# Kernel tuning notes

Measured on AMD Instinct MI355X. Metric: run time of the kernel, lower is better.

The kernel has to match this reference:

```python
import jax, jax.numpy as jnp
import numpy as np

B, N, K, D = 16, 8192, 20, 64  # batch, points, neighbors, feature dim
LN_EPS = 1e-5


def setup_inputs() -> dict:
    key = jax.random.key(0)
    k1, k2, k3 = jax.random.split(key, 3)
    x = jax.random.normal(k1, (B, N, D), dtype=jnp.float32)
    neighbor_ind = jax.random.randint(k2, (B, N, K), 0, N)
    # torch Linear(2D -> D, bias=False): weight shape (out=D, in=2D), y = feat @ W.T
    W = jax.random.normal(k3, (D, 2 * D), dtype=jnp.float32) * (1.0 / np.sqrt(2 * D))
    gamma = jnp.ones((D,), jnp.float32)
    beta = jnp.zeros((D,), jnp.float32)
    return {"x": x, "neighbor_ind": neighbor_ind, "W": W, "gamma": gamma, "beta": beta}


def reference(x, neighbor_ind, W, gamma, beta):
    # route(): gather neighbor features and build [neighbor - center, center]
    neighbor_x = jax.vmap(lambda xb, ib: xb[ib])(x, neighbor_ind)        # (b, n, k, d)
    center = x[:, :, None, :]                                            # (b, n, 1, d)
    feat = jnp.concatenate(
        [neighbor_x - center, jnp.broadcast_to(center, neighbor_x.shape)], axis=-1
    )                                                                    # (b, n, k, 2d)
    # per-edge Linear (bias=False), then max over k neighbors
    h = jnp.einsum('bnke,oe->bnko', feat, W)                             # (b, n, k, d)
    h = h.max(axis=2)                                                    # (b, n, d)
    # LayerNorm over last dim, then exact GELU
    mu = h.mean(axis=-1, keepdims=True)
    var = jnp.mean((h - mu) ** 2, axis=-1, keepdims=True)
    hn = (h - mu) * jax.lax.rsqrt(var + LN_EPS) * gamma + beta
    return jax.nn.gelu(hn, approximate=False)
```

## Files before the change

### kernel.cpp

```cpp
#include <hip/hip_runtime.h>
#include <math.h>

#define B_ 16
#define N_ 8192
#define K_ 20
#define NPTS (B_ * N_)

typedef __attribute__((ext_vector_type(4))) float f4;
typedef __attribute__((ext_vector_type(8))) short s8;
typedef __attribute__((ext_vector_type(4))) unsigned int u4;
typedef __attribute__((ext_vector_type(4))) unsigned short us4;

__device__ __forceinline__ unsigned short f2bf(float f) {
    union { float f; unsigned u; } v; v.f = f;
    return (unsigned short)((v.u + 0x7FFFu + ((v.u >> 16) & 1u)) >> 16);
}
__device__ __forceinline__ float bfhi(unsigned w) { return __uint_as_float(w & 0xFFFF0000u); }
__device__ __forceinline__ float bflo(unsigned w) { return __uint_as_float(w << 16); }

__global__ __launch_bounds__(256) void prep_kernel(const float* __restrict__ W,
                                                   unsigned short* __restrict__ Wg) {
    const int i = blockIdx.x * 256 + threadIdx.x;
    const int j = i >> 6, d = i & 63;
    const float v = (j < 64) ? W[j * 128 + d]
                             : (W[(j - 64) * 128 + 64 + d] - W[(j - 64) * 128 + d]);
    Wg[i] = f2bf(v);
}

__global__ __launch_bounds__(256) void proj_kernel(const float* __restrict__ x,
                                                   const unsigned short* __restrict__ Wg,
                                                   unsigned short* __restrict__ Y1,
                                                   unsigned short* __restrict__ Bs) {
    __shared__ unsigned short Wl[128 * 72];
    const int t = threadIdx.x;

    for (int i = t; i < 1024; i += 256) {
        u4 v = ((const u4*)Wg)[i];
        *((u4*)((char*)Wl + (i >> 3) * 144 + (i & 7) * 16)) = v;
    }
    __syncthreads();

    const int lane = t & 63;
    const int wv = t >> 6;
    const int m = lane & 15;
    const int q = lane >> 4;
    const int pbase = blockIdx.x * 64 + wv * 16;

    const float* xr = x + (size_t)(pbase + m) * 64 + q * 8;
    f4 x0 = *(const f4*)(xr);
    f4 x1 = *(const f4*)(xr + 4);
    f4 x2 = *(const f4*)(xr + 32);
    f4 x3 = *(const f4*)(xr + 36);
    s8 X0, X1;
    X0[0]=(short)f2bf(x0.x); X0[1]=(short)f2bf(x0.y); X0[2]=(short)f2bf(x0.z); X0[3]=(short)f2bf(x0.w);
    X0[4]=(short)f2bf(x1.x); X0[5]=(short)f2bf(x1.y); X0[6]=(short)f2bf(x1.z); X0[7]=(short)f2bf(x1.w);
    X1[0]=(short)f2bf(x2.x); X1[1]=(short)f2bf(x2.y); X1[2]=(short)f2bf(x2.z); X1[3]=(short)f2bf(x2.w);
    X1[4]=(short)f2bf(x3.x); X1[5]=(short)f2bf(x3.y); X1[6]=(short)f2bf(x3.z); X1[7]=(short)f2bf(x3.w);

    f4 acc[8];
#pragma unroll
    for (int tt = 0; tt < 8; ++tt) acc[tt] = (f4)0.f;

#pragma unroll
    for (int s = 0; s < 2; ++s) {
        const s8 X = s ? X1 : X0;
#pragma unroll
        for (int tt = 0; tt < 8; ++tt) {
            s8 w = *(const s8*)((const char*)Wl + (16 * tt + m) * 144 + s * 64 + q * 16);
            acc[tt] = __builtin_amdgcn_mfma_f32_16x16x32_bf16(w, X, acc[tt], 0, 0, 0);
        }
    }

    const size_t prow = (size_t)(pbase + m) * 64;
#pragma unroll
    for (int tt = 0; tt < 4; ++tt) {
        us4 u;
        u.x = f2bf(acc[tt][0]); u.y = f2bf(acc[tt][1]);
        u.z = f2bf(acc[tt][2]); u.w = f2bf(acc[tt][3]);
        *(us4*)&Y1[prow + tt * 16 + q * 4] = u;
    }
#pragma unroll
    for (int tt = 4; tt < 8; ++tt) {
        us4 u;
        u.x = f2bf(acc[tt][0]); u.y = f2bf(acc[tt][1]);
        u.z = f2bf(acc[tt][2]); u.w = f2bf(acc[tt][3]);
        *(us4*)&Bs[prow + (tt - 4) * 16 + q * 4] = u;
    }
}

__global__ __launch_bounds__(256) void gather_kernel(const unsigned short* __restrict__ Y1,
                                                     const unsigned short* __restrict__ Bs,
                                                     const int* __restrict__ ind,
                                                     const float* __restrict__ gamma,
                                                     const float* __restrict__ beta,
                                                     float* __restrict__ out) {
    const int lane = threadIdx.x & 63;
    const int wave = threadIdx.x >> 6;
    const int sub = lane & 7;
    const int q = lane >> 3;
    const int bi = blockIdx.x;
    const int bt = bi & 15;
    const int jj = bi >> 4;
    const int p = bt * N_ + jj * 32 + wave * 8 + q;
    const int bbase = bt * N_ * 64;

    int idxs[K_];
    const int4* ip = (const int4*)&ind[p * K_];
#pragma unroll
    for (int v = 0; v < 5; ++v) {
        int4 iv = ip[v];
        idxs[4 * v + 0] = iv.x; idxs[4 * v + 1] = iv.y;
        idxs[4 * v + 2] = iv.z; idxs[4 * v + 3] = iv.w;
    }

    f4 ma = (f4)(-INFINITY), mb = (f4)(-INFINITY);
#pragma unroll
    for (int r = 0; r < 2; ++r) {
        u4 rv[10];
#pragma unroll
        for (int k = 0; k < 10; ++k)
            rv[k] = *(const u4*)(Y1 + bbase + idxs[r * 10 + k] * 64 + sub * 8);
#pragma unroll
        for (int k = 0; k < 10; ++k) {
            ma.x = fmaxf(ma.x, bflo(rv[k].x)); ma.y = fmaxf(ma.y, bfhi(rv[k].x));
            ma.z = fmaxf(ma.z, bflo(rv[k].y)); ma.w = fmaxf(ma.w, bfhi(rv[k].y));
            mb.x = fmaxf(mb.x, bflo(rv[k].z)); mb.y = fmaxf(mb.y, bfhi(rv[k].z));
            mb.z = fmaxf(mb.z, bflo(rv[k].w)); mb.w = fmaxf(mb.w, bfhi(rv[k].w));
        }
    }

    u4 bsv = __builtin_nontemporal_load((const u4*)(Bs + (size_t)p * 64 + sub * 8));
    f4 ha, hb;
    ha.x = ma.x + bflo(bsv.x); ha.y = ma.y + bfhi(bsv.x);
    ha.z = ma.z + bflo(bsv.y); ha.w = ma.w + bfhi(bsv.y);
    hb.x = mb.x + bflo(bsv.z); hb.y = mb.y + bfhi(bsv.z);
    hb.z = mb.z + bflo(bsv.w); hb.w = mb.w + bfhi(bsv.w);

    float s = ha.x + ha.y + ha.z + ha.w + hb.x + hb.y + hb.z + hb.w;
#pragma unroll
    for (int off = 4; off >= 1; off >>= 1) s += __shfl_xor(s, off, 64);
    const float mu = s * (1.0f / 64.0f);
    f4 da = ha - mu, db = hb - mu;
    float v2 = da.x * da.x + da.y * da.y + da.z * da.z + da.w * da.w
             + db.x * db.x + db.y * db.y + db.z * db.z + db.w * db.w;
#pragma unroll
    for (int off = 4; off >= 1; off >>= 1) v2 += __shfl_xor(v2, off, 64);
    const float rstd = rsqrtf(v2 * (1.0f / 64.0f) + 1e-5f);

    const f4 g0 = *(const f4*)&gamma[sub * 8];
    const f4 g1 = *(const f4*)&gamma[sub * 8 + 4];
    const f4 b0 = *(const f4*)&beta[sub * 8];
    const f4 b1 = *(const f4*)&beta[sub * 8 + 4];
    f4 na = da * rstd * g0 + b0;
    f4 nb = db * rstd * g1 + b1;

    f4 r0, r1;
    r0.x = 0.5f * na.x * (1.0f + erff(na.x * 0.70710678f));
    r0.y = 0.5f * na.y * (1.0f + erff(na.y * 0.70710678f));
    r0.z = 0.5f * na.z * (1.0f + erff(na.z * 0.70710678f));
    r0.w = 0.5f * na.w * (1.0f + erff(na.w * 0.70710678f));
    r1.x = 0.5f * nb.x * (1.0f + erff(nb.x * 0.70710678f));
    r1.y = 0.5f * nb.y * (1.0f + erff(nb.y * 0.70710678f));
    r1.z = 0.5f * nb.z * (1.0f + erff(nb.z * 0.70710678f));
    r1.w = 0.5f * nb.w * (1.0f + erff(nb.w * 0.70710678f));
    float* op = &out[(size_t)p * 64 + sub * 8];
    __builtin_nontemporal_store(r0, (f4*)op);
    __builtin_nontemporal_store(r1, (f4*)(op + 4));
}

extern "C" void kernel_launch(void* const* d_in, const int* in_sizes, int n_in,
                              void* d_out, int out_size, void* d_ws, size_t ws_size,
                              hipStream_t stream) {
    const float* x     = (const float*)d_in[0];
    const int*   ind   = (const int*)d_in[1];
    const float* W     = (const float*)d_in[2];
    const float* gamma = (const float*)d_in[3];
    const float* beta  = (const float*)d_in[4];
    float* out = (float*)d_out;

    unsigned short* Bs = (unsigned short*)d_ws;
    unsigned short* Y1 = Bs + (size_t)NPTS * 64;
    unsigned short* Wg = Y1 + (size_t)NPTS * 64;

    prep_kernel<<<32, 256, 0, stream>>>(W, Wg);
    proj_kernel<<<NPTS / 64, 256, 0, stream>>>(x, Wg, Y1, Bs);
    gather_kernel<<<NPTS / 32, 256, 0, stream>>>(Y1, Bs, ind, gamma, beta, out);
}
```

Before: 125.6 us.

## Fuse prep, projection and gather into one cooperative persistent kernel

Replaces the three launches with one cooperative kernel of 512 blocks. Each block builds the bf16 weight fragments in registers, projects 256 points, keeps the center term in shared memory, and writes only the neighbor table Y1 to global memory. A grid-wide sync then lets the same block gather, max-reduce (using v_max3), LayerNorm and apply GELU for its points. This removes two launch gaps and the global round trip of the center term, at the cost of a grid barrier and fewer resident blocks. The old three-kernel path is kept as a fallback if the cooperative launch fails.

New measurement: 216.3 us. 72.1% more time.

```diff
diff --git a/kernel.cpp b/kernel.cpp
--- a/kernel.cpp
+++ b/kernel.cpp
@@ -1,4 +1,5 @@
 #include <hip/hip_runtime.h>
+#include <hip/hip_cooperative_groups.h>
 #include <math.h>
 
 #define B_ 16
@@ -10,6 +11,7 @@
 typedef __attribute__((ext_vector_type(8))) short s8;
 typedef __attribute__((ext_vector_type(4))) unsigned int u4;
 typedef __attribute__((ext_vector_type(4))) unsigned short us4;
+typedef __attribute__((ext_vector_type(4))) int i4;
 
 __device__ __forceinline__ unsigned short f2bf(float f) {
     union { float f; unsigned u; } v; v.f = f;
@@ -17,6 +19,181 @@
 }
 __device__ __forceinline__ float bfhi(unsigned w) { return __uint_as_float(w & 0xFFFF0000u); }
 __device__ __forceinline__ float bflo(unsigned w) { return __uint_as_float(w << 16); }
+__device__ __forceinline__ float max3f(float a, float b, float c) {
+    float d;
+    asm("v_max3_f32 %0, %1, %2, %3" : "=v"(d) : "v"(a), "v"(b), "v"(c));
+    return d;
+}
+
+__global__ __launch_bounds__(256, 3) void fused_kernel(
+    const float* __restrict__ x, const int* __restrict__ ind,
+    const float* __restrict__ W, const float* __restrict__ gamma,
+    const float* __restrict__ beta, float* __restrict__ out,
+    unsigned short* __restrict__ Y1)
+{
+    __shared__ unsigned short BsL[256 * 72];
+
+    const int t = threadIdx.x;
+    const int lane = t & 63, wv = t >> 6;
+    const int g = blockIdx.x;
+    const int b = (g & 7) + 8 * ((g >> 3) & 1);
+    const int z = g >> 4;
+    const int p0 = b * N_ + z * 256;
+
+    const int mm = lane & 15, qq = lane >> 4;
+    s8 wf[16];
+#pragma unroll
+    for (int tt = 0; tt < 8; ++tt) {
+#pragma unroll
+        for (int s = 0; s < 2; ++s) {
+            const int k0 = s * 32 + qq * 8;
+            s8 w;
+            if (tt < 4) {
+                const int row = 16 * tt + mm;
+                f4 a0 = *(const f4*)&W[row * 128 + k0];
+                f4 a1 = *(const f4*)&W[row * 128 + k0 + 4];
+                w[0]=(short)f2bf(a0.x); w[1]=(short)f2bf(a0.y);
+                w[2]=(short)f2bf(a0.z); w[3]=(short)f2bf(a0.w);
+                w[4]=(short)f2bf(a1.x); w[5]=(short)f2bf(a1.y);
+                w[6]=(short)f2bf(a1.z); w[7]=(short)f2bf(a1.w);
+            } else {
+                const int row = 16 * (tt - 4) + mm;
+                f4 a0 = *(const f4*)&W[row * 128 + 64 + k0];
+                f4 a1 = *(const f4*)&W[row * 128 + 64 + k0 + 4];
+                f4 c0 = *(const f4*)&W[row * 128 + k0];
+                f4 c1 = *(const f4*)&W[row * 128 + k0 + 4];
+                w[0]=(short)f2bf(a0.x-c0.x); w[1]=(short)f2bf(a0.y-c0.y);
+                w[2]=(short)f2bf(a0.z-c0.z); w[3]=(short)f2bf(a0.w-c0.w);
+                w[4]=(short)f2bf(a1.x-c1.x); w[5]=(short)f2bf(a1.y-c1.y);
+                w[6]=(short)f2bf(a1.z-c1.z); w[7]=(short)f2bf(a1.w-c1.w);
+            }
+            wf[tt * 2 + s] = w;
+        }
+    }
+
+#pragma unroll 2
+    for (int tile = 0; tile < 4; ++tile) {
+        const int plocal = tile * 64 + wv * 16 + mm;
+        const int pg = p0 + plocal;
+        const float* xr = x + (size_t)pg * 64 + qq * 8;
+        f4 x0 = __builtin_nontemporal_load((const f4*)xr);
+        f4 x1 = __builtin_nontemporal_load((const f4*)(xr + 4));
+        f4 x2 = __builtin_nontemporal_load((const f4*)(xr + 32));
+        f4 x3 = __builtin_nontemporal_load((const f4*)(xr + 36));
+        s8 X0, X1;
+        X0[0]=(short)f2bf(x0.x); X0[1]=(short)f2bf(x0.y); X0[2]=(short)f2bf(x0.z); X0[3]=(short)f2bf(x0.w);
+        X0[4]=(short)f2bf(x1.x); X0[5]=(short)f2bf(x1.y); X0[6]=(short)f2bf(x1.z); X0[7]=(short)f2bf(x1.w);
+        X1[0]=(short)f2bf(x2.x); X1[1]=(short)f2bf(x2.y); X1[2]=(short)f2bf(x2.z); X1[3]=(short)f2bf(x2.w);
+        X1[4]=(short)f2bf(x3.x); X1[5]=(short)f2bf(x3.y); X1[6]=(short)f2bf(x3.z); X1[7]=(short)f2bf(x3.w);
+
+        f4 acc[8];
+#pragma unroll
+        for (int tt = 0; tt < 8; ++tt) acc[tt] = (f4)0.f;
+#pragma unroll
+        for (int s = 0; s < 2; ++s) {
+            const s8 X = s ? X1 : X0;
+#pragma unroll
+            for (int tt = 0; tt < 8; ++tt)
+                acc[tt] = __builtin_amdgcn_mfma_f32_16x16x32_bf16(wf[tt * 2 + s], X, acc[tt], 0, 0, 0);
+        }
+
+        const size_t prow = (size_t)pg * 64;
+#pragma unroll
+        for (int tt = 0; tt < 4; ++tt) {
+            us4 u;
+            u.x = f2bf(acc[tt][0]); u.y = f2bf(acc[tt][1]);
+            u.z = f2bf(acc[tt][2]); u.w = f2bf(acc[tt][3]);
+            __builtin_nontemporal_store(u, (us4*)&Y1[prow + tt * 16 + qq * 4]);
+        }
+#pragma unroll
+        for (int tt = 4; tt < 8; ++tt) {
+            us4 u;
+            u.x = f2bf(acc[tt][0]); u.y = f2bf(acc[tt][1]);
+            u.z = f2bf(acc[tt][2]); u.w = f2bf(acc[tt][3]);
+            *(us4*)((char*)BsL + plocal * 144 + (tt - 4) * 32 + qq * 8) = u;
+        }
+    }
+
+    cooperative_groups::this_grid().sync();
+
+    const int sub = lane & 7;
+    const int qp = lane >> 3;
+    const f4 g0 = *(const f4*)&gamma[sub * 8];
+    const f4 g1 = *(const f4*)&gamma[sub * 8 + 4];
+    const f4 be0 = *(const f4*)&beta[sub * 8];
+    const f4 be1 = *(const f4*)&beta[sub * 8 + 4];
+    const unsigned short* tbl = Y1 + (size_t)b * (N_ * 64) + sub * 8;
+
+#pragma unroll 1
+    for (int pass = 0; pass < 8; ++pass) {
+        const int pl = pass * 32 + wv * 8 + qp;
+        const int pg = p0 + pl;
+
+        int idxs[K_];
+        const i4* ip = (const i4*)&ind[pg * K_];
+#pragma unroll
+        for (int v = 0; v < 5; ++v) {
+            i4 iv = __builtin_nontemporal_load(ip + v);
+            idxs[4 * v + 0] = iv.x; idxs[4 * v + 1] = iv.y;
+            idxs[4 * v + 2] = iv.z; idxs[4 * v + 3] = iv.w;
+        }
+
+        f4 ma = (f4)(-INFINITY), mb = (f4)(-INFINITY);
+#pragma unroll
+        for (int r = 0; r < 2; ++r) {
+            u4 rv[10];
+#pragma unroll
+            for (int k = 0; k < 10; ++k)
+                rv[k] = *(const u4*)(tbl + idxs[r * 10 + k] * 64);
+#pragma unroll
+            for (int k = 0; k < 10; k += 2) {
+                u4 a = rv[k], c = rv[k + 1];
+                ma.x = max3f(ma.x, bflo(a.x), bflo(c.x));
+                ma.y = max3f(ma.y, bfhi(a.x), bfhi(c.x));
+                ma.z = max3f(ma.z, bflo(a.y), bflo(c.y));
+                ma.w = max3f(ma.w, bfhi(a.y), bfhi(c.y));
+                mb.x = max3f(mb.x, bflo(a.z), bflo(c.z));
+                mb.y = max3f(mb.y, bfhi(a.z), bfhi(c.z));
+                mb.z = max3f(mb.z, bflo(a.w), bflo(c.w));
+                mb.w = max3f(mb.w, bfhi(a.w), bfhi(c.w));
+            }
+        }
+
+        const u4 bsv = *(const u4*)((const char*)BsL + pl * 144 + sub * 16);
+        f4 ha, hb;
+        ha.x = ma.x + bflo(bsv.x); ha.y = ma.y + bfhi(bsv.x);
+        ha.z = ma.z + bflo(bsv.y); ha.w = ma.w + bfhi(bsv.y);
+        hb.x = mb.x + bflo(bsv.z); hb.y = mb.y + bfhi(bsv.z);
+        hb.z = mb.z + bflo(bsv.w); hb.w = mb.w + bfhi(bsv.w);
+
+        float s = ha.x + ha.y + ha.z + ha.w + hb.x + hb.y + hb.z + hb.w;
+#pragma unroll
+        for (int off = 4; off >= 1; off >>= 1) s += __shfl_xor(s, off, 64);
+        const float mu = s * (1.0f / 64.0f);
+        f4 da = ha - mu, db = hb - mu;
+        float v2 = da.x * da.x + da.y * da.y + da.z * da.z + da.w * da.w
+                 + db.x * db.x + db.y * db.y + db.z * db.z + db.w * db.w;
+#pragma unroll
+        for (int off = 4; off >= 1; off >>= 1) v2 += __shfl_xor(v2, off, 64);
+        const float rstd = rsqrtf(v2 * (1.0f / 64.0f) + 1e-5f);
+
+        f4 na = da * rstd * g0 + be0;
+        f4 nb = db * rstd * g1 + be1;
+
+        f4 r0, r1;
+        r0.x = 0.5f * na.x * (1.0f + erff(na.x * 0.70710678f));
+        r0.y = 0.5f * na.y * (1.0f + erff(na.y * 0.70710678f));
+        r0.z = 0.5f * na.z * (1.0f + erff(na.z * 0.70710678f));
+        r0.w = 0.5f * na.w * (1.0f + erff(na.w * 0.70710678f));
+        r1.x = 0.5f * nb.x * (1.0f + erff(nb.x * 0.70710678f));
+        r1.y = 0.5f * nb.y * (1.0f + erff(nb.y * 0.70710678f));
+        r1.z = 0.5f * nb.z * (1.0f + erff(nb.z * 0.70710678f));
+        r1.w = 0.5f * nb.w * (1.0f + erff(nb.w * 0.70710678f));
+        float* op = &out[(size_t)pg * 64 + sub * 8];
+        __builtin_nontemporal_store(r0, (f4*)op);
+        __builtin_nontemporal_store(r1, (f4*)(op + 4));
+    }
+}
 
 __global__ __launch_bounds__(256) void prep_kernel(const float* __restrict__ W,
                                                    unsigned short* __restrict__ Wg) {
@@ -182,7 +359,13 @@
     unsigned short* Y1 = Bs + (size_t)NPTS * 64;
     unsigned short* Wg = Y1 + (size_t)NPTS * 64;
 
-    prep_kernel<<<32, 256, 0, stream>>>(W, Wg);
-    proj_kernel<<<NPTS / 64, 256, 0, stream>>>(x, Wg, Y1, Bs);
-    gather_kernel<<<NPTS / 32, 256, 0, stream>>>(Y1, Bs, ind, gamma, beta, out);
-}
+    void* args[] = {(void*)&x, (void*)&ind, (void*)&W, (void*)&gamma,
+                    (void*)&beta, (void*)&out, (void*)&Y1};
+    hipError_t e = hipLaunchCooperativeKernel((const void*)fused_kernel,
+                                              dim3(512), dim3(256), args, 0, stream);
+    if (e != hipSuccess) {
+        prep_kernel<<<32, 256, 0, stream>>>(W, Wg);
+        proj_kernel<<<NPTS / 64, 256, 0, stream>>>(x, Wg, Y1, Bs);
+        gather_kernel<<<NPTS / 32, 256, 0, stream>>>(Y1, Bs, ind, gamma, beta, out);
+    }
+}
```
